# Kernel tuning notes

Hardware: AMD Instinct MI355X
Metric: run time of the kernel (lower is better)

Reference implementation:

```python
import jax, jax.numpy as jnp
import numpy as np

IMG = 100          # IMG_SIZE
NQ = 4             # N_QUBITS
STEP = 2           # sqrt(NQ)
NP_SIDE = IMG // STEP   # 50 patches per side
NPATCH = NP_SIDE * NP_SIDE  # 2500

# Fixed surrogate for tq.RandomLayer(n_ops=8): 6 param rotations + 2 CNOTs
OPS = [("rx", 0), ("ry", 1), ("rz", 2), ("cnot", (0, 1)),
       ("rx", 3), ("cnot", (2, 3)), ("ry", 0), ("rz", 1)]


def _apply_1q(psi, G, w):
    # psi: [N,2,2,2,2] complex, G: [2,2] complex, wire w
    out = jnp.tensordot(G, psi, axes=[[1], [w + 1]])  # new wire axis at 0
    return jnp.moveaxis(out, 0, w + 1)


def _apply_cnot(psi, c, t):
    p0 = jax.lax.index_in_dim(psi, 0, axis=c + 1, keepdims=True)
    p1 = jax.lax.index_in_dim(psi, 1, axis=c + 1, keepdims=True)
    p1 = jnp.flip(p1, axis=t + 1)  # X on target when control=1
    return jnp.concatenate([p0, p1], axis=c + 1)


def _gate(name, t):
    tc = t.astype(jnp.complex64)
    c, s = jnp.cos(tc / 2), jnp.sin(tc / 2)
    if name == "rx":
        return jnp.stack([jnp.stack([c, -1j * s]), jnp.stack([-1j * s, c])])
    if name == "ry":
        return jnp.stack([jnp.stack([c, -s]), jnp.stack([s, c])])
    # rz
    em, ep = jnp.exp(-0.5j * tc), jnp.exp(0.5j * tc)
    z = jnp.zeros_like(em)
    return jnp.stack([jnp.stack([em, z]), jnp.stack([z, ep])])


def _quanv(x, q_params):
    # x: [B,100,100] -> batched 4-qubit statevector sim over all patches
    B = x.shape[0]
    # patch pixel order: [x[c,r], x[c,r+1], x[c+1,r], x[c+1,r+1]]
    p = x.reshape(B, NP_SIDE, STEP, NP_SIDE, STEP)
    p = p.transpose(0, 1, 3, 2, 4).reshape(B * NPATCH, NQ)  # [N,4] angles
    half = 0.5 * p
    a = jnp.stack([jnp.cos(half), jnp.sin(half)], axis=-1)  # [N,4,2] RY|0>
    psi = jnp.einsum("na,nb,nc,nd->nabcd", a[:, 0], a[:, 1], a[:, 2], a[:, 3])
    psi = psi.astype(jnp.complex64)
    pi = 0
    for name, w in OPS:
        if name == "cnot":
            psi = _apply_cnot(psi, w[0], w[1])
        else:
            psi = _apply_1q(psi, _gate(name, q_params[pi]), w)
            pi += 1
    probs = jnp.abs(psi) ** 2  # [N,2,2,2,2] real
    zsign = jnp.array([1.0, -1.0], dtype=probs.dtype)
    exps = []
    for w in range(NQ):
        zb = zsign.reshape((1,) + (1,) * w + (2,) + (1,) * (NQ - 1 - w))
        exps.append((probs * zb).sum(axis=(1, 2, 3, 4)))
    meas = jnp.stack(exps, axis=-1)  # [N,4] PauliZ expvals
    return meas.reshape(B, NPATCH * NQ).astype(jnp.float32)  # [B,10000]


def setup_inputs() -> dict:
    key = jax.random.key(0)
    k1, k2, k3, k4 = jax.random.split(key, 4)
    x = jax.random.uniform(k1, (64, IMG, IMG), dtype=jnp.float32)
    W = jax.random.normal(k2, (2, IMG * IMG), dtype=jnp.float32) * 0.01
    b = jax.random.normal(k3, (2,), dtype=jnp.float32) * 0.01
    q_params = jax.random.uniform(k4, (6,), dtype=jnp.float32) * 2.0 * np.pi
    return {"x": x, "W": W, "b": b, "q_params": q_params}


def reference(x, W, b, q_params):
    feats = jax.lax.stop_gradient(_quanv(x, q_params))  # torch.no_grad() block
    logits = feats @ W.T + b
    return jax.nn.log_softmax(logits, axis=-1)
```

## Files before the change

kernel.cpp:

```cpp
#include <hip/hip_runtime.h>
#include <math.h>

#define IMG      100
#define NPS      50
#define NPATCH   2500
#define NIMG     64
#define BLK      1024


__global__ __launch_bounds__(BLK) void quanv_fused_kernel(
    const float* __restrict__ x,
    const float* __restrict__ W,
    const float* __restrict__ bias,
    const float* __restrict__ qp,
    float* __restrict__ out)
{
    const int b = blockIdx.x;

    float gc[6], gs[6];
    #pragma unroll
    for (int k = 0; k < 6; ++k) {
        __sincosf(0.5f * qp[k], &gs[k], &gc[k]);
    }

    float t0 = 0.0f, t1 = 0.0f;

    for (int p = threadIdx.x; p < NPATCH; p += BLK) {
        const int pi = p / NPS;
        const int pj = p - pi * NPS;
        const float* xb = x + b * (IMG * IMG) + (2 * pi) * IMG + 2 * pj;
        float ang0 = xb[0];
        float ang1 = xb[1];
        float ang2 = xb[IMG];
        float ang3 = xb[IMG + 1];

        float ca[4], sa[4];
        __sincosf(0.5f * ang0, &sa[0], &ca[0]);
        __sincosf(0.5f * ang1, &sa[1], &ca[1]);
        __sincosf(0.5f * ang2, &sa[2], &ca[2]);
        __sincosf(0.5f * ang3, &sa[3], &ca[3]);

        float2 psi[16];
        #pragma unroll
        for (int i = 0; i < 16; ++i) {
            float v = ((i & 8) ? sa[0] : ca[0]) *
                      ((i & 4) ? sa[1] : ca[1]) *
                      ((i & 2) ? sa[2] : ca[2]) *
                      ((i & 1) ? sa[3] : ca[3]);
            psi[i] = make_float2(v, 0.0f);
        }

        #define APPLY_RX(m, c, s)                                              \
            _Pragma("unroll")                                                  \
            for (int i = 0; i < 16; ++i) if (!(i & (m))) {                     \
                int j = i | (m);                                               \
                float2 p0 = psi[i], p1 = psi[j];                               \
                psi[i] = make_float2((c)*p0.x + (s)*p1.y,                      \
                                     (c)*p0.y - (s)*p1.x);                     \
                psi[j] = make_float2((s)*p0.y + (c)*p1.x,                      \
                                    -(s)*p0.x + (c)*p1.y);                     \
            }

        #define APPLY_RY(m, c, s)                                              \
            _Pragma("unroll")                                                  \
            for (int i = 0; i < 16; ++i) if (!(i & (m))) {                     \
                int j = i | (m);                                               \
                float2 p0 = psi[i], p1 = psi[j];                               \
                psi[i] = make_float2((c)*p0.x - (s)*p1.x,                      \
                                     (c)*p0.y - (s)*p1.y);                     \
                psi[j] = make_float2((s)*p0.x + (c)*p1.x,                      \
                                     (s)*p0.y + (c)*p1.y);                     \
            }

        #define APPLY_RZ(m, c, s)                                              \
            _Pragma("unroll")                                                  \
            for (int i = 0; i < 16; ++i) {                                     \
                float2 pp = psi[i];                                            \
                if (i & (m)) {                                                 \
                    psi[i] = make_float2((c)*pp.x - (s)*pp.y,                  \
                                         (c)*pp.y + (s)*pp.x);                 \
                } else {                                                       \
                    psi[i] = make_float2((c)*pp.x + (s)*pp.y,                  \
                                         (c)*pp.y - (s)*pp.x);                 \
                }                                                              \
            }

        #define APPLY_CNOT(mc, mt)                                             \
            _Pragma("unroll")                                                  \
            for (int i = 0; i < 16; ++i) if ((i & (mc)) && !(i & (mt))) {      \
                int j = i | (mt);                                              \
                float2 tmp = psi[i]; psi[i] = psi[j]; psi[j] = tmp;            \
            }

        APPLY_RX(8, gc[0], gs[0]);
        APPLY_RY(4, gc[1], gs[1]);
        APPLY_RZ(2, gc[2], gs[2]);
        APPLY_CNOT(8, 4);
        APPLY_RX(1, gc[3], gs[3]);
        APPLY_CNOT(2, 1);
        APPLY_RY(8, gc[4], gs[4]);
        APPLY_RZ(4, gc[5], gs[5]);

        float e0 = 0.f, e1 = 0.f, e2 = 0.f, e3 = 0.f;
        #pragma unroll
        for (int i = 0; i < 16; ++i) {
            float pr = psi[i].x * psi[i].x + psi[i].y * psi[i].y;
            e0 += (i & 8) ? -pr : pr;
            e1 += (i & 4) ? -pr : pr;
            e2 += (i & 2) ? -pr : pr;
            e3 += (i & 1) ? -pr : pr;
        }

        const float4 w0 = reinterpret_cast<const float4*>(W)[p];
        const float4 w1 = reinterpret_cast<const float4*>(W)[NPATCH + p];
        t0 += e0 * w0.x + e1 * w0.y + e2 * w0.z + e3 * w0.w;
        t1 += e0 * w1.x + e1 * w1.y + e2 * w1.z + e3 * w1.w;
    }

    #pragma unroll
    for (int off = 32; off > 0; off >>= 1) {
        t0 += __shfl_down(t0, off);
        t1 += __shfl_down(t1, off);
    }
    __shared__ float red0[BLK / 64], red1[BLK / 64];
    const int lane = threadIdx.x & 63;
    const int wv   = threadIdx.x >> 6;
    if (lane == 0) { red0[wv] = t0; red1[wv] = t1; }
    __syncthreads();
    if (threadIdx.x == 0) {
        float l0 = 0.f, l1 = 0.f;
        #pragma unroll
        for (int w = 0; w < BLK / 64; ++w) { l0 += red0[w]; l1 += red1[w]; }
        l0 += bias[0];
        l1 += bias[1];
        float m   = fmaxf(l0, l1);
        float lse = m + logf(__expf(l0 - m) + __expf(l1 - m));
        out[b * 2 + 0] = l0 - lse;
        out[b * 2 + 1] = l1 - lse;
    }
}

extern "C" void kernel_launch(void* const* d_in, const int* in_sizes, int n_in,
                              void* d_out, int out_size, void* d_ws, size_t ws_size,
                              hipStream_t stream) {
    const float* x    = (const float*)d_in[0];
    const float* W    = (const float*)d_in[1];
    const float* bias = (const float*)d_in[2];
    const float* qp   = (const float*)d_in[3];
    float* out = (float*)d_out;

    quanv_fused_kernel<<<NIMG, BLK, 0, stream>>>(x, W, bias, qp, out);
}
```

Before: 66.10 us.

## Replace statevector simulation with closed-form Pauli-Z expectation formulas

The per-patch 16-amplitude complex statevector simulation is replaced with analytically derived closed-form expressions for the four PauliZ expectations, built from the input angles and precomputed products of the gate-parameter cosines and sines. Pixel loads are also merged into two float2 loads per patch. This removes most of the per-patch arithmetic and register pressure. The risk is that any error in the derivation gives wrong results, and the formulas are tied to the fixed gate sequence.

```diff
diff --git a/kernel.cpp b/kernel.cpp
--- a/kernel.cpp
+++ b/kernel.cpp
@@ -17,99 +17,40 @@
 {
     const int b = blockIdx.x;
 
-    float gc[6], gs[6];
-    #pragma unroll
-    for (int k = 0; k < 6; ++k) {
-        __sincosf(0.5f * qp[k], &gs[k], &gc[k]);
-    }
+    const float C0 = __cosf(qp[0]);
+    float S1, C1;  __sincosf(qp[1], &S1, &C1);
+    const float C3 = __cosf(qp[3]);
+    float S4, C4;  __sincosf(qp[4], &S4, &C4);
+
+    const float k_a = C0 * C4;
+    const float k_b = S4 * C1;
+    const float k_c = S4 * S1;
+    const float k_d = C0 * C1;
+    const float k_e = C0 * S1;
+    const float k_f = C3;
 
     float t0 = 0.0f, t1 = 0.0f;
+
+    const float* xb = x + b * (IMG * IMG);
 
     for (int p = threadIdx.x; p < NPATCH; p += BLK) {
         const int pi = p / NPS;
         const int pj = p - pi * NPS;
-        const float* xb = x + b * (IMG * IMG) + (2 * pi) * IMG + 2 * pj;
-        float ang0 = xb[0];
-        float ang1 = xb[1];
-        float ang2 = xb[IMG];
-        float ang3 = xb[IMG + 1];
 
-        float ca[4], sa[4];
-        __sincosf(0.5f * ang0, &sa[0], &ca[0]);
-        __sincosf(0.5f * ang1, &sa[1], &ca[1]);
-        __sincosf(0.5f * ang2, &sa[2], &ca[2]);
-        __sincosf(0.5f * ang3, &sa[3], &ca[3]);
+        const float2 r0 = *reinterpret_cast<const float2*>(xb + (2 * pi) * IMG + 2 * pj);
+        const float2 r1 = *reinterpret_cast<const float2*>(xb + (2 * pi + 1) * IMG + 2 * pj);
+        const float x0 = r0.x, x1 = r0.y, x2 = r1.x, x3 = r1.y;
 
-        float2 psi[16];
-        #pragma unroll
-        for (int i = 0; i < 16; ++i) {
-            float v = ((i & 8) ? sa[0] : ca[0]) *
-                      ((i & 4) ? sa[1] : ca[1]) *
-                      ((i & 2) ? sa[2] : ca[2]) *
-                      ((i & 1) ? sa[3] : ca[3]);
-            psi[i] = make_float2(v, 0.0f);
-        }
+        float sx0, cz0, sx1, cz1;
+        __sincosf(x0, &sx0, &cz0);
+        __sincosf(x1, &sx1, &cz1);
+        const float cz2 = __cosf(x2);
+        const float cz3 = __cosf(x3);
 
-        #define APPLY_RX(m, c, s)                                              \
-            _Pragma("unroll")                                                  \
-            for (int i = 0; i < 16; ++i) if (!(i & (m))) {                     \
-                int j = i | (m);                                               \
-                float2 p0 = psi[i], p1 = psi[j];                               \
-                psi[i] = make_float2((c)*p0.x + (s)*p1.y,                      \
-                                     (c)*p0.y - (s)*p1.x);                     \
-                psi[j] = make_float2((s)*p0.y + (c)*p1.x,                      \
-                                    -(s)*p0.x + (c)*p1.y);                     \
-            }
-
-        #define APPLY_RY(m, c, s)                                              \
-            _Pragma("unroll")                                                  \
-            for (int i = 0; i < 16; ++i) if (!(i & (m))) {                     \
-                int j = i | (m);                                               \
-                float2 p0 = psi[i], p1 = psi[j];                               \
-                psi[i] = make_float2((c)*p0.x - (s)*p1.x,                      \
-                                     (c)*p0.y - (s)*p1.y);                     \
-                psi[j] = make_float2((s)*p0.x + (c)*p1.x,                      \
-                                     (s)*p0.y + (c)*p1.y);                     \
-            }
-
-        #define APPLY_RZ(m, c, s)                                              \
-            _Pragma("unroll")                                                  \
-            for (int i = 0; i < 16; ++i) {                                     \
-                float2 pp = psi[i];                                            \
-                if (i & (m)) {                                                 \
-                    psi[i] = make_float2((c)*pp.x - (s)*pp.y,                  \
-                                         (c)*pp.y + (s)*pp.x);                 \
-                } else {                                                       \
-                    psi[i] = make_float2((c)*pp.x + (s)*pp.y,                  \
-                                         (c)*pp.y - (s)*pp.x);                 \
-                }                                                              \
-            }
-
-        #define APPLY_CNOT(mc, mt)                                             \
-            _Pragma("unroll")                                                  \
-            for (int i = 0; i < 16; ++i) if ((i & (mc)) && !(i & (mt))) {      \
-                int j = i | (mt);                                              \
-                float2 tmp = psi[i]; psi[i] = psi[j]; psi[j] = tmp;            \
-            }
-
-        APPLY_RX(8, gc[0], gs[0]);
-        APPLY_RY(4, gc[1], gs[1]);
-        APPLY_RZ(2, gc[2], gs[2]);
-        APPLY_CNOT(8, 4);
-        APPLY_RX(1, gc[3], gs[3]);
-        APPLY_CNOT(2, 1);
-        APPLY_RY(8, gc[4], gs[4]);
-        APPLY_RZ(4, gc[5], gs[5]);
-
-        float e0 = 0.f, e1 = 0.f, e2 = 0.f, e3 = 0.f;
-        #pragma unroll
-        for (int i = 0; i < 16; ++i) {
-            float pr = psi[i].x * psi[i].x + psi[i].y * psi[i].y;
-            e0 += (i & 8) ? -pr : pr;
-            e1 += (i & 4) ? -pr : pr;
-            e2 += (i & 2) ? -pr : pr;
-            e3 += (i & 1) ? -pr : pr;
-        }
+        const float e0 = k_a * cz0 - k_b * sx0 * sx1 - k_c * sx0 * cz1;
+        const float e1 = k_d * cz0 * cz1 - k_e * cz0 * sx1;
+        const float e2 = cz2;
+        const float e3 = k_f * cz2 * cz3;
 
         const float4 w0 = reinterpret_cast<const float4*>(W)[p];
         const float4 w1 = reinterpret_cast<const float4*>(W)[NPATCH + p];
```

Measured after the change: 60.97 us. -7.8%, faster.
